# Kernel optimization log

Hardware: AMD Instinct MI355X
Metric: run time of the kernel (lower is better)

## Reference

```python
import jax, jax.numpy as jnp
import numpy as np
from jax import lax

IN_FEATURES = 1024
CLASSES = 512
OUT_CHANNELS = 32
N = 4096
CONV1_OUT = 32
K = 3


def setup_inputs() -> dict:
    key = jax.random.key(0)
    ks = jax.random.split(key, 7)
    s_lin = 1.0 / np.sqrt(IN_FEATURES)
    s_c1 = 1.0 / np.sqrt(1 * K)
    s_c2 = 1.0 / np.sqrt(CONV1_OUT * K)
    return {
        "x": jax.random.normal(ks[0], (N, IN_FEATURES), dtype=jnp.float32),
        "W_w": jax.random.uniform(ks[1], (CLASSES, IN_FEATURES), jnp.float32, -s_lin, s_lin),
        "W_b": jax.random.uniform(ks[2], (CLASSES,), jnp.float32, -s_lin, s_lin),
        "conv1_w": jax.random.uniform(ks[3], (CONV1_OUT, 1, K), jnp.float32, -s_c1, s_c1),
        "conv1_b": jax.random.uniform(ks[4], (CONV1_OUT,), jnp.float32, -s_c1, s_c1),
        "conv2_w": jax.random.uniform(ks[5], (OUT_CHANNELS, CONV1_OUT, K), jnp.float32, -s_c2, s_c2),
        "conv2_b": jax.random.uniform(ks[6], (OUT_CHANNELS,), jnp.float32, -s_c2, s_c2),
    }


def _conv1d(x, w, b):
    # x: [N, C_in, L], w: [C_out, C_in, K], padding=1 (same)
    y = lax.conv_general_dilated(
        x, w, window_strides=(1,), padding=((1, 1),),
        dimension_numbers=("NCH", "OIH", "NCH"))
    return y + b[None, :, None]


def reference(x, W_w, W_b, conv1_w, conv1_b, conv2_w, conv2_b):
    # SelfAttention: h = x W^T + b  -> [N, CLASSES]
    h = x @ W_w.T + W_b
    # attention = softmax(tanh(h h^T), dim=1)  -> [N, N]
    scores = jnp.tanh(h @ h.T)
    attn = jax.nn.softmax(scores, axis=1)
    a = jnp.tanh(attn @ h)                     # [N, CLASSES]
    a = jax.nn.relu(a)
    # unsqueeze(-1).permute(0,2,1): [N, CLASSES] -> [N, 1, CLASSES]
    z = a[:, None, :]
    z = jax.nn.relu(_conv1d(z, conv1_w, conv1_b))   # [N, 32, CLASSES]
    z = jax.nn.relu(_conv1d(z, conv2_w, conv2_b))   # [N, OUT_CHANNELS, CLASSES]
    return jnp.transpose(z, (0, 2, 1))              # [N, CLASSES, OUT_CHANNELS]
```

## Files before the change

kernel.cpp:

```cpp
#include <hip/hip_runtime.h>

typedef __bf16 bf16_t;
typedef __bf16 bf16x8 __attribute__((ext_vector_type(8)));
typedef __bf16 bf16x4v __attribute__((ext_vector_type(4)));
typedef __bf16 bf16x2 __attribute__((ext_vector_type(2)));
typedef float f32x4 __attribute__((ext_vector_type(4)));

__device__ __forceinline__ float tanh_fast(float x) {
  float a = fabsf(x);
  float e = __expf(-2.f * a);
  float t = (1.f - e) * __builtin_amdgcn_rcpf(1.f + e);
  return copysignf(t, x);
}

__device__ __forceinline__ void gload16(const void* g, void* l) {
  __builtin_amdgcn_global_load_lds(
      (const __attribute__((address_space(1))) void*)g,
      (__attribute__((address_space(3))) void*)l, 16, 0, 0);
}

__global__ __launch_bounds__(256) void cast_all_k(const float* __restrict__ x,
                                                  const float* __restrict__ Ww,
                                                  const float* __restrict__ w2,
                                                  bf16_t* __restrict__ xb,
                                                  bf16_t* __restrict__ Wbf,
                                                  bf16_t* __restrict__ w2rg) {
  const int bid = blockIdx.x;
  const int tid = threadIdx.x;
  if (bid < 4096) {
    const int i = bid * 256 + tid;
    float4 v = ((const float4*)x)[i];
    bf16x4v o;
    o[0] = (bf16_t)v.x; o[1] = (bf16_t)v.y; o[2] = (bf16_t)v.z; o[3] = (bf16_t)v.w;
    ((bf16x4v*)xb)[i] = o;
  } else if (bid < 4608) {
    const int i = (bid - 4096) * 256 + tid;
    float4 v = ((const float4*)Ww)[i];
    bf16x4v o;
    o[0] = (bf16_t)v.x; o[1] = (bf16_t)v.y; o[2] = (bf16_t)v.z; o[3] = (bf16_t)v.w;
    ((bf16x4v*)Wbf)[i] = o;
  } else {
    for (int i = tid; i < 3072; i += 256) {
      int o = i / 96, rem = i % 96, c = rem / 3, kk = rem % 3;
      w2rg[kk * 1024 + o * 32 + c] = (bf16_t)w2[i];
    }
  }
}

#define BAR() __builtin_amdgcn_s_barrier()
#define WLG() asm volatile("s_waitcnt lgkmcnt(0)" ::: "memory")
#define RDA(b, am)                                                              \
  do {                                                                          \
    _Pragma("unroll") for (int j = 0; j < 4; ++j) {                             \
      afr[j][0] = *(const bf16x8*)(pA + (b)*16384 + (am)*4096 + j*1024);        \
      afr[j][1] = *(const bf16x8*)(pA + (b)*16384 + 8192 + (am)*4096 + j*1024); \
    }                                                                           \
  } while (0)
#define RDB(b, bn)                                                              \
  do {                                                                          \
    _Pragma("unroll") for (int jj = 0; jj < 2; ++jj) {                          \
      bfr[jj][0] = *(const bf16x8*)(pB + (b)*16384 + ((bn)*2+jj)*1024);         \
      bfr[jj][1] = *(const bf16x8*)(pB + (b)*16384 + 8192 + ((bn)*2+jj)*1024);  \
    }                                                                           \
  } while (0)
#define MM16(am, bn)                                                            \
  do {                                                                          \
    __builtin_amdgcn_s_setprio(1);                                              \
    _Pragma("unroll") for (int kk = 0; kk < 2; ++kk)                            \
    _Pragma("unroll") for (int j = 0; j < 4; ++j)                               \
    _Pragma("unroll") for (int jj = 0; jj < 2; ++jj)                            \
      acc[(am)*4+j][(bn)*2+jj] = __builtin_amdgcn_mfma_f32_16x16x32_bf16(       \
          afr[j][kk], bfr[jj][kk], acc[(am)*4+j][(bn)*2+jj], 0, 0, 0);          \
    __builtin_amdgcn_s_setprio(0);                                              \
  } while (0)
#define STGA(tile, half)                                                        \
  do {                                                                          \
    const bf16_t* s_ = Ag + (size_t)(half)*128*lda + (tile)*64;                 \
    char* d_ = lds_raw + (half)*32768 + ((tile)&1)*16384 + tid*16;              \
    gload16(s_, d_); gload16(s_ + 32, d_ + 8192);                               \
  } while (0)
#define STGB(tile, half)                                                        \
  do {                                                                          \
    const bf16_t* s_ = Bg + (size_t)(half)*128*ldb + (tile)*64;                 \
    char* d_ = lds_raw + 65536 + (half)*32768 + ((tile)&1)*16384 + tid*16;      \
    gload16(s_, d_); gload16(s_ + 32, d_ + 8192);                               \
  } while (0)

template <int EPI>
__global__ __launch_bounds__(512, 2) void gemm8_k(const bf16_t* __restrict__ A,
                                                  const bf16_t* __restrict__ Bt,
                                                  bf16_t* __restrict__ out,
                                                  float* __restrict__ psum,
                                                  int lda, int ldb, int ldc,
                                                  int Klen, size_t pstride) {
  __shared__ __attribute__((aligned(16))) char lds_raw[131072];
  const int tid = threadIdx.x;
  const int wid = tid >> 6, l = tid & 63;
  const int wm = wid >> 2, wn = wid & 3;
  const int lr = l & 15, lkq = l >> 4;

  const int gx = gridDim.x, gy = gridDim.y;
  const int flat = blockIdx.x + gx * (blockIdx.y + gy * blockIdx.z);
  const int n = gx * gy * gridDim.z;
  const int s = (flat & 7) * (n >> 3) + (flat >> 3);
  const int lgx = __builtin_ctz(gx), lgy = __builtin_ctz(gy);
  const int bx = s & (gx - 1);
  const int by = (s >> lgx) & (gy - 1);
  const int bz = s >> (lgx + lgy);

  const size_t koff = (size_t)bz * Klen;
  const int NI = Klen >> 7;

  const int srow = tid >> 2;
  const int scol = ((tid & 3) * 8) ^ (((tid >> 5) & 1) << 4);
  const bf16_t* Ag = A + (size_t)(by * 256 + srow) * lda + koff + scol;
  const bf16_t* Bg = Bt + (size_t)(bx * 256 + srow) * ldb + koff + scol;

  const int kby = (lkq * 16) ^ (((lr >> 3) & 1) << 5);
  const char* pA = lds_raw + wm * 32768 + lr * 64 + kby;
  const char* pB = lds_raw + 65536 + (wn >> 1) * 32768 + ((wn & 1) * 64 + lr) * 64 + kby;

  bf16x8 afr[4][2], bfr[2][2];
  f32x4 acc[8][4];
#pragma unroll
  for (int m = 0; m < 8; ++m)
#pragma unroll
    for (int n2 = 0; n2 < 4; ++n2) acc[m][n2] = (f32x4){0.f, 0.f, 0.f, 0.f};

  STGA(0, 0); STGA(0, 1); STGB(0, 0); STGB(0, 1); STGA(1, 0);

  for (int i = 0; i < NI; ++i) {
    const int t1 = 2 * i + 1, t2 = 2 * i + 2, t3 = 2 * i + 3;
    const bool more = (i + 1 < NI);
    asm volatile("s_waitcnt vmcnt(2)" ::: "memory");
    BAR();
    RDA(0, 0); RDB(0, 0);
    STGA(t1, 1);
    WLG(); MM16(0, 0); BAR();
    RDB(0, 1); STGB(t1, 0);
    BAR(); WLG(); MM16(0, 1); BAR();
    RDA(0, 1); STGB(t1, 1);
    BAR(); WLG(); MM16(1, 1); BAR();
    RDB(0, 0);
    if (more) STGA(t2, 0);
    BAR(); WLG(); MM16(1, 0); BAR();
    if (more) { asm volatile("s_waitcnt vmcnt(2)" ::: "memory"); }
    else      { asm volatile("s_waitcnt vmcnt(0)" ::: "memory"); }
    BAR();
    RDA(1, 0); RDB(1, 0);
    if (more) STGA(t2, 1);
    WLG(); MM16(0, 0); BAR();
    RDB(1, 1);
    if (more) STGB(t2, 0);
    BAR(); WLG(); MM16(0, 1); BAR();
    RDA(1, 1);
    if (more) STGB(t2, 1);
    BAR(); WLG(); MM16(1, 1); BAR();
    RDB(1, 0);
    if (more) STGA(t3, 0);
    BAR(); WLG(); MM16(1, 0); BAR();
  }

  if constexpr (EPI == 1) {
    float* ps = psum + (size_t)(bx * 4 + wn) * 4096;
#pragma unroll
    for (int mi = 0; mi < 8; ++mi) {
#pragma unroll
      for (int v = 0; v < 4; ++v) {
        const int r = wm * 128 + mi * 16 + lkq * 4 + v;
        float rs = 0.f;
#pragma unroll
        for (int ni = 0; ni < 4; ++ni) {
          float val = __expf(tanh_fast(acc[mi][ni][v]));
          const int cb = ((wn * 64 + ni * 16 + lr) * 2) ^ ((r & 4) << 4);
          *(bf16_t*)(lds_raw + r * 512 + cb) = (bf16_t)val;
          rs += val;
        }
        rs += __shfl_xor(rs, 1);
        rs += __shfl_xor(rs, 2);
        rs += __shfl_xor(rs, 4);
        rs += __shfl_xor(rs, 8);
        if (lr == 0) ps[by * 256 + r] = rs;
      }
    }
  } else {
#pragma unroll
    for (int mi = 0; mi < 8; ++mi)
#pragma unroll
      for (int v = 0; v < 4; ++v) {
        const int r = wm * 128 + mi * 16 + lkq * 4 + v;
#pragma unroll
        for (int ni = 0; ni < 4; ++ni) {
          const int cb = ((wn * 64 + ni * 16 + lr) * 2) ^ ((r & 4) << 4);
          *(bf16_t*)(lds_raw + r * 512 + cb) = (bf16_t)acc[mi][ni][v];
        }
      }
  }
  __syncthreads();
  bf16_t* obase = (EPI == 1) ? out : out + (size_t)bz * pstride;
#pragma unroll
  for (int k = 0; k < 16; ++k) {
    const int idx = k * 512 + tid;
    const int row = idx >> 5, cc = idx & 31;
    bf16x8 vv = *(const bf16x8*)(lds_raw + ((row * 512 + cc * 16) ^ ((row & 4) << 4)));
    *(bf16x8*)&obase[(size_t)(by * 256 + row) * ldc + bx * 256 + cc * 8] = vv;
  }
}

template <int EPI>
__global__ __launch_bounds__(256) void gemm_bt_k(const bf16_t* __restrict__ A,
                                                 const bf16_t* __restrict__ Bt,
                                                 const float* __restrict__ extra,
                                                 bf16_t* __restrict__ out,
                                                 float* __restrict__ outf,
                                                 float* __restrict__ psum,
                                                 int M, int N, int Kloop, int lda, int ldb) {
  __shared__ bf16_t As[128 * 32];
  __shared__ bf16_t Bs[128 * 32];
  const int tid = threadIdx.x;
  const int w = tid >> 6;
  const int l = tid & 63;
  const int bx = blockIdx.x, by = blockIdx.y;
  const int koff = blockIdx.z * Kloop;

  const bf16_t* src = (w < 2) ? A : Bt;
  const int stride = (w < 2) ? lda : ldb;
  bf16_t* dstbase = (w < 2) ? As : Bs;
  const int tile0 = (w < 2 ? by : bx) * 128 + (w & 1) * 64;
  const int srow = l >> 2;
  const int scol = (l & 3) * 8;
  const bf16_t* gbase = src + (size_t)(tile0 + srow) * stride + scol + koff;
  bf16_t* lbase = dstbase + (w & 1) * (64 * 32);

  const int wm = w >> 1, wn = w & 1;
  const int lrow = l & 15;
  const int lk = (l >> 4) * 8;

  f32x4 zero = {0.f, 0.f, 0.f, 0.f};
  f32x4 acc[4][4];
  for (int m = 0; m < 4; ++m)
    for (int n = 0; n < 4; ++n) acc[m][n] = zero;

  for (int kt = 0; kt < Kloop; kt += 32) {
    const bf16_t* g = gbase + kt;
#pragma unroll
    for (int i = 0; i < 4; ++i) gload16(g + (size_t)i * 16 * stride, lbase + i * 512);
    __syncthreads();
    bf16x8 af[4], bfv[4];
#pragma unroll
    for (int m = 0; m < 4; ++m)
      af[m] = *(const bf16x8*)&As[(wm * 64 + m * 16 + lrow) * 32 + lk];
#pragma unroll
    for (int n = 0; n < 4; ++n)
      bfv[n] = *(const bf16x8*)&Bs[(wn * 64 + n * 16 + lrow) * 32 + lk];
#pragma unroll
    for (int m = 0; m < 4; ++m)
#pragma unroll
      for (int n = 0; n < 4; ++n)
        acc[m][n] = __builtin_amdgcn_mfma_f32_16x16x32_bf16(af[m], bfv[n], acc[m][n], 0, 0, 0);
    __syncthreads();
  }

  const int row0 = by * 128 + wm * 64;
  const int col0 = bx * 128 + wn * 64;

  if constexpr (EPI == 3) {
    float* of = outf + (size_t)blockIdx.z * M * N;
#pragma unroll
    for (int m = 0; m < 4; ++m)
#pragma unroll
      for (int v = 0; v < 4; ++v) {
        const int row = row0 + m * 16 + ((l >> 4) << 2) + v;
#pragma unroll
        for (int n = 0; n < 4; ++n)
          of[(size_t)row * N + col0 + n * 16 + lrow] = acc[m][n][v];
      }
    return;
  }

  if constexpr (EPI == 1) {
#pragma unroll
    for (int m = 0; m < 4; ++m)
#pragma unroll
      for (int v = 0; v < 4; ++v) {
        const int row = row0 + m * 16 + ((l >> 4) << 2) + v;
        float rs = 0.f;
#pragma unroll
        for (int n = 0; n < 4; ++n) {
          const int col = col0 + n * 16 + lrow;
          float val = __expf(tanh_fast(acc[m][n][v]));
          out[(size_t)row * N + col] = (bf16_t)val;
          rs += val;
        }
        if (psum) {
          rs += __shfl_xor(rs, 1);
          rs += __shfl_xor(rs, 2);
          rs += __shfl_xor(rs, 4);
          rs += __shfl_xor(rs, 8);
          if ((l & 15) == 0) psum[(size_t)(bx * 2 + wn) * M + row] = rs;
        }
      }
    return;
  }

  float bcol[4];
#pragma unroll
  for (int n = 0; n < 4; ++n)
    bcol[n] = (EPI == 0) ? extra[col0 + n * 16 + lrow] : 0.f;

#pragma unroll
  for (int m = 0; m < 4; ++m) {
#pragma unroll
    for (int v = 0; v < 4; ++v) {
      const int row = row0 + m * 16 + ((l >> 4) << 2) + v;
      float inv_dn = 1.f;
      if constexpr (EPI == 2) inv_dn = 1.f / extra[row];
#pragma unroll
      for (int n = 0; n < 4; ++n) {
        const int col = col0 + n * 16 + lrow;
        float val = acc[m][n][v];
        float o;
        if constexpr (EPI == 0) o = val + bcol[n];
        else o = fmaxf(tanh_fast(val * inv_dn), 0.f);
        out[(size_t)row * N + col] = (bf16_t)o;
      }
    }
  }
}

__global__ __launch_bounds__(256) void reduce1T_k(const float* __restrict__ p0,
                                                  const float* __restrict__ p1,
                                                  const float* __restrict__ bias,
                                                  bf16_t* __restrict__ h,
                                                  bf16_t* __restrict__ hT) {
  __shared__ bf16_t tile[64][65];
  const int d0 = blockIdx.x * 64;
  const int i0 = blockIdx.y * 64;
  const int tid = threadIdx.x;
#pragma unroll
  for (int p = 0; p < 2; ++p) {
    const int r = p * 32 + (tid >> 3);
    const int c8 = (tid & 7) * 8;
    const size_t idx = (size_t)(i0 + r) * 512 + d0 + c8;
    float4 a0 = *(const float4*)&p0[idx];
    float4 a1 = *(const float4*)&p0[idx + 4];
    float4 b0 = *(const float4*)&p1[idx];
    float4 b1 = *(const float4*)&p1[idx + 4];
    float4 w0 = *(const float4*)&bias[d0 + c8];
    float4 w1 = *(const float4*)&bias[d0 + c8 + 4];
    bf16x8 o;
    o[0] = (bf16_t)(a0.x + b0.x + w0.x);
    o[1] = (bf16_t)(a0.y + b0.y + w0.y);
    o[2] = (bf16_t)(a0.z + b0.z + w0.z);
    o[3] = (bf16_t)(a0.w + b0.w + w0.w);
    o[4] = (bf16_t)(a1.x + b1.x + w1.x);
    o[5] = (bf16_t)(a1.y + b1.y + w1.y);
    o[6] = (bf16_t)(a1.z + b1.z + w1.z);
    o[7] = (bf16_t)(a1.w + b1.w + w1.w);
    *(bf16x8*)&h[idx] = o;
#pragma unroll
    for (int k = 0; k < 8; ++k) tile[r][c8 + k] = o[k];
  }
  __syncthreads();
#pragma unroll
  for (int p = 0; p < 2; ++p) {
    const int d = p * 32 + (tid >> 3);
    const int i8 = (tid & 7) * 8;
    bf16x8 u;
#pragma unroll
    for (int k = 0; k < 8; ++k) u[k] = tile[i8 + k][d];
    *(bf16x8*)&hT[(size_t)(d0 + d) * 4096 + i0 + i8] = u;
  }
}

__global__ __launch_bounds__(256) void transpose_k(const bf16_t* __restrict__ h,
                                                   bf16_t* __restrict__ hT) {
  __shared__ bf16_t tile[64][65];
  const int i0 = blockIdx.x * 64;
  const int d0 = blockIdx.y * 64;
  const int tid = threadIdx.x;
#pragma unroll
  for (int p = 0; p < 2; ++p) {
    int r = p * 32 + (tid >> 3);
    int c8 = (tid & 7) * 8;
    bf16x8 v = *(const bf16x8*)&h[(size_t)(i0 + r) * 512 + d0 + c8];
#pragma unroll
    for (int k = 0; k < 8; ++k) tile[r][c8 + k] = v[k];
  }
  __syncthreads();
#pragma unroll
  for (int p = 0; p < 2; ++p) {
    int d = p * 32 + (tid >> 3);
    int i8 = (tid & 7) * 8;
    bf16x8 u;
#pragma unroll
    for (int k = 0; k < 8; ++k) u[k] = tile[i8 + k][d];
    *(bf16x8*)&hT[(size_t)(d0 + d) * 4096 + i0 + i8] = u;
  }
}

__global__ __launch_bounds__(256) void rowsum_k(const bf16_t* __restrict__ P,
                                                float* __restrict__ den) {
  const int r = blockIdx.x;
  const int tid = threadIdx.x;
  const bf16_t* p = P + (size_t)r * 4096 + tid * 16;
  bf16x8 a = *(const bf16x8*)p;
  bf16x8 b = *(const bf16x8*)(p + 8);
  float s = 0.f;
#pragma unroll
  for (int k = 0; k < 8; ++k) s += (float)a[k] + (float)b[k];
  __shared__ float red[256];
  red[tid] = s;
  __syncthreads();
  for (int off = 128; off > 0; off >>= 1) {
    if (tid < off) red[tid] += red[tid + off];
    __syncthreads();
  }
  if (tid == 0) den[r] = red[0];
}

__global__ __launch_bounds__(256) void conv2_fused_k(const bf16_t* __restrict__ pg,
                                                     const float* __restrict__ psum,
                                                     const bf16_t* __restrict__ w2rg,
                                                     const float* __restrict__ w1,
                                                     const float* __restrict__ b1,
                                                     const float* __restrict__ b2,
                                                     float* __restrict__ out, int S) {
  __shared__ bf16_t trow[516];
  __shared__ bf16_t z1t[514 * 40];
  __shared__ bf16_t w2r[3072];
  __shared__ float w1s[96], b1s[32], b2s[32];
  __shared__ float den_s;
  const int r = blockIdx.x;
  const int tid = threadIdx.x;

  if (tid < 96) w1s[tid] = w1[tid];
  if (tid < 32) { b1s[tid] = b1[tid]; b2s[tid] = b2[tid]; }
  ((bf16x8*)w2r)[tid] = ((const bf16x8*)w2rg)[tid];
  if (tid < 128) ((bf16x8*)w2r)[256 + tid] = ((const bf16x8*)w2rg)[256 + tid];

  if (tid < 64) {
    float dp = psum[(size_t)tid * 4096 + r];
    dp += __shfl_xor(dp, 32);
    dp += __shfl_xor(dp, 16);
    dp += __shfl_xor(dp, 8);
    dp += __shfl_xor(dp, 4);
    dp += __shfl_xor(dp, 2);
    dp += __shfl_xor(dp, 1);
    if (tid == 0) den_s = dp;
  }

  float a0 = 0.f, a1 = 0.f;
  {
    const bf16_t* pr = pg + (size_t)r * 512 + tid * 2;
    for (int z = 0; z < S; ++z) {
      bf16x2 v = *(const bf16x2*)(pr + (size_t)z * (4096 * 512));
      a0 += (float)v[0];
      a1 += (float)v[1];
    }
  }
  if (tid == 0) { trow[0] = (bf16_t)0.f; trow[513] = (bf16_t)0.f; }
  if (tid < 40) { z1t[tid] = (bf16_t)0.f; z1t[513 * 40 + tid] = (bf16_t)0.f; }
  __syncthreads();

  {
    const float inv = 1.f / den_s;
    trow[1 + 2 * tid] = (bf16_t)fmaxf(tanh_fast(a0 * inv), 0.f);
    trow[2 + 2 * tid] = (bf16_t)fmaxf(tanh_fast(a1 * inv), 0.f);
  }
  __syncthreads();

  {
    const int c = tid & 31;
    const int jb = (tid >> 5) * 64;
    const float wc0 = w1s[c * 3], wc1 = w1s[c * 3 + 1], wc2 = w1s[c * 3 + 2];
    const float bb = b1s[c];
    float tm = (float)trow[jb];
    float t0 = (float)trow[jb + 1];
    for (int j = jb; j < jb + 64; ++j) {
      float tp2 = (float)trow[j + 2];
      float v = fmaxf(bb + wc0 * tm + wc1 * t0 + wc2 * tp2, 0.f);
      z1t[(j + 1) * 40 + c] = (bf16_t)v;
      tm = t0; t0 = tp2;
    }
  }
  __syncthreads();

  const int w = tid >> 6, l = tid & 63;
  const int lrow = l & 15;
  const int lk = (l >> 4) * 8;
  bf16x8 af[3][2];
#pragma unroll
  for (int kk = 0; kk < 3; ++kk)
#pragma unroll
    for (int m = 0; m < 2; ++m)
      af[kk][m] = *(const bf16x8*)&w2r[kk * 1024 + (m * 16 + lrow) * 32 + lk];

  f32x4 zero = {0.f, 0.f, 0.f, 0.f};
  f32x4 acc[2][8];
#pragma unroll
  for (int m = 0; m < 2; ++m)
#pragma unroll
    for (int n = 0; n < 8; ++n) acc[m][n] = zero;

  const int j0 = w * 128;
#pragma unroll
  for (int kk = 0; kk < 3; ++kk) {
#pragma unroll
    for (int n = 0; n < 8; ++n) {
      bf16x8 bfv = *(const bf16x8*)&z1t[(j0 + n * 16 + lrow + kk) * 40 + lk];
      acc[0][n] = __builtin_amdgcn_mfma_f32_16x16x32_bf16(af[kk][0], bfv, acc[0][n], 0, 0, 0);
      acc[1][n] = __builtin_amdgcn_mfma_f32_16x16x32_bf16(af[kk][1], bfv, acc[1][n], 0, 0, 0);
    }
  }

#pragma unroll
  for (int m = 0; m < 2; ++m) {
    const int ob = m * 16 + ((l >> 4) << 2);
    const float bb0 = b2s[ob], bb1 = b2s[ob + 1], bb2 = b2s[ob + 2], bb3 = b2s[ob + 3];
#pragma unroll
    for (int n = 0; n < 8; ++n) {
      const int j = j0 + n * 16 + lrow;
      f32x4 res;
      res[0] = fmaxf(acc[m][n][0] + bb0, 0.f);
      res[1] = fmaxf(acc[m][n][1] + bb1, 0.f);
      res[2] = fmaxf(acc[m][n][2] + bb2, 0.f);
      res[3] = fmaxf(acc[m][n][3] + bb3, 0.f);
      *(f32x4*)&out[((size_t)r * 512 + j) * 32 + ob] = res;
    }
  }
}

__global__ __launch_bounds__(256) void conv_fused_k(const bf16_t* __restrict__ t,
                                                    const float* __restrict__ w1,
                                                    const float* __restrict__ b1,
                                                    const float* __restrict__ w2,
                                                    const float* __restrict__ b2,
                                                    float* __restrict__ out) {
  __shared__ bf16_t trow[516];
  __shared__ bf16_t z1t[514 * 40];
  __shared__ bf16_t w2r[3 * 32 * 32];
  __shared__ float w1s[96], b1s[32], b2s[32];
  const int r = blockIdx.x;
  const int tid = threadIdx.x;

  if (tid < 96) w1s[tid] = w1[tid];
  if (tid < 32) { b1s[tid] = b1[tid]; b2s[tid] = b2[tid]; }
  for (int i = tid; i < 3072; i += 256) {
    int o = i / 96, rem = i % 96, c = rem / 3, kk = rem % 3;
    w2r[kk * 1024 + o * 32 + c] = (bf16_t)w2[i];
  }
  {
    const bf16_t* tp = t + (size_t)r * 512;
    trow[1 + tid] = tp[tid];
    trow[1 + 256 + tid] = tp[256 + tid];
    if (tid == 0) { trow[0] = (bf16_t)0.f; trow[513] = (bf16_t)0.f; }
    if (tid < 40) { z1t[tid] = (bf16_t)0.f; z1t[513 * 40 + tid] = (bf16_t)0.f; }
  }
  __syncthreads();

  {
    const int c = tid & 31;
    const int jb = (tid >> 5) * 64;
    const float wc0 = w1s[c * 3], wc1 = w1s[c * 3 + 1], wc2 = w1s[c * 3 + 2];
    const float bb = b1s[c];
    float tm = (float)trow[jb];
    float t0 = (float)trow[jb + 1];
    for (int j = jb; j < jb + 64; ++j) {
      float tp2 = (float)trow[j + 2];
      float v = fmaxf(bb + wc0 * tm + wc1 * t0 + wc2 * tp2, 0.f);
      z1t[(j + 1) * 40 + c] = (bf16_t)v;
      tm = t0; t0 = tp2;
    }
  }
  __syncthreads();

  const int w = tid >> 6, l = tid & 63;
  const int lrow = l & 15;
  const int lk = (l >> 4) * 8;
  bf16x8 af[3][2];
#pragma unroll
  for (int kk = 0; kk < 3; ++kk)
#pragma unroll
    for (int m = 0; m < 2; ++m)
      af[kk][m] = *(const bf16x8*)&w2r[kk * 1024 + (m * 16 + lrow) * 32 + lk];

  f32x4 zero = {0.f, 0.f, 0.f, 0.f};
  f32x4 acc[2][8];
#pragma unroll
  for (int m = 0; m < 2; ++m)
#pragma unroll
    for (int n = 0; n < 8; ++n) acc[m][n] = zero;

  const int j0 = w * 128;
#pragma unroll
  for (int kk = 0; kk < 3; ++kk) {
#pragma unroll
    for (int n = 0; n < 8; ++n) {
      bf16x8 bfv = *(const bf16x8*)&z1t[(j0 + n * 16 + lrow + kk) * 40 + lk];
      acc[0][n] = __builtin_amdgcn_mfma_f32_16x16x32_bf16(af[kk][0], bfv, acc[0][n], 0, 0, 0);
      acc[1][n] = __builtin_amdgcn_mfma_f32_16x16x32_bf16(af[kk][1], bfv, acc[1][n], 0, 0, 0);
    }
  }

#pragma unroll
  for (int m = 0; m < 2; ++m) {
    const int ob = m * 16 + ((l >> 4) << 2);
    const float bb0 = b2s[ob], bb1 = b2s[ob + 1], bb2 = b2s[ob + 2], bb3 = b2s[ob + 3];
#pragma unroll
    for (int n = 0; n < 8; ++n) {
      const int j = j0 + n * 16 + lrow;
      f32x4 res;
      res[0] = fmaxf(acc[m][n][0] + bb0, 0.f);
      res[1] = fmaxf(acc[m][n][1] + bb1, 0.f);
      res[2] = fmaxf(acc[m][n][2] + bb2, 0.f);
      res[3] = fmaxf(acc[m][n][3] + bb3, 0.f);
      *(f32x4*)&out[((size_t)r * 512 + j) * 32 + ob] = res;
    }
  }
}

extern "C" void kernel_launch(void* const* d_in, const int* in_sizes, int n_in,
                              void* d_out, int out_size, void* d_ws, size_t ws_size,
                              hipStream_t stream) {
  const float* x = (const float*)d_in[0];
  const float* Ww = (const float*)d_in[1];
  const float* Wb = (const float*)d_in[2];
  const float* c1w = (const float*)d_in[3];
  const float* c1b = (const float*)d_in[4];
  const float* c2w = (const float*)d_in[5];
  const float* c2b = (const float*)d_in[6];
  float* out = (float*)d_out;
  char* ws = (char*)d_ws;

  bf16_t* xb  = (bf16_t*)(ws + 0);
  bf16_t* Wbf = (bf16_t*)(ws + 8388608);
  bf16_t* h   = (bf16_t*)(ws + 9437184);
  bf16_t* hT  = (bf16_t*)(ws + 13631488);
  bf16_t* tb  = (bf16_t*)(ws + 17825792);
  bf16_t* w2rg = (bf16_t*)(ws + 17825792);
  float*  den = (float*)(ws + 22020096);

  cast_all_k<<<4609, 256, 0, stream>>>(x, Ww, c2w, xb, Wbf, w2rg);

  const size_t NEED_FAST = 73416704ull;
  if (ws_size >= NEED_FAST) {
    float*  psum = (float*)(ws + 22036480);
    bf16_t* P    = (bf16_t*)(ws + 23085056);
    float*  pg1  = (float*)(ws + 23085056);
    bf16_t* pg3b = (bf16_t*)(ws + 56639488);

    gemm_bt_k<3><<<dim3(4, 32, 2), 256, 0, stream>>>(xb, Wbf, nullptr, nullptr, pg1,
                                                     nullptr, 4096, 512, 512, 1024, 1024);
    reduce1T_k<<<dim3(8, 64), 256, 0, stream>>>(pg1, pg1 + 4096 * 512, Wb, h, hT);

    gemm8_k<1><<<dim3(16, 16, 1), 512, 0, stream>>>(h, h, P, psum, 512, 512, 4096, 512, 0);

    const int S = (ws_size >= 90193920ull) ? 8 : 4;
    gemm8_k<3><<<dim3(2, 16, S), 512, 0, stream>>>(P, hT, pg3b, nullptr, 4096, 4096, 512,
                                                   4096 / S, (size_t)4096 * 512);

    conv2_fused_k<<<4096, 256, 0, stream>>>(pg3b, psum, w2rg, c1w, c1b, c2b, out, S);
  } else {
    bf16_t* P = (bf16_t*)(ws + 22036480);
    gemm_bt_k<0><<<dim3(4, 32), 256, 0, stream>>>(xb, Wbf, Wb, h, nullptr, nullptr,
                                                  4096, 512, 1024, 1024, 1024);
    transpose_k<<<dim3(64, 8), 256, 0, stream>>>(h, hT);
    gemm_bt_k<1><<<dim3(32, 32), 256, 0, stream>>>(h, h, nullptr, P, nullptr, nullptr,
                                                   4096, 4096, 512, 512, 512);
    rowsum_k<<<4096, 256, 0, stream>>>(P, den);
    gemm_bt_k<2><<<dim3(4, 32), 256, 0, stream>>>(P, hT, den, tb, nullptr, nullptr,
                                                  4096, 512, 4096, 4096, 4096);
    conv_fused_k<<<4096, 256, 0, stream>>>(tb, c1w, c1b, c2w, c2b, out);
  }
}
```

Before: 182.9 us.

## Exploit symmetry of h·hᵀ and split conv epilogue into half-row blocks

The scores GEMM now computes only the upper-triangular 256x256 tiles (136 blocks instead of 256). Each off-diagonal tile writes its transpose to P and column partial sums into psum, which roughly halves the MFMA work for that GEMM. The conv kernel is split into two blocks per row with halo handling, using less LDS and requesting 4 blocks per CU for higher occupancy. The risks are uncoalesced transposed-tile writes from scalar LDS gathers and the extra halo recomputation.

```diff
diff --git a/kernel.cpp b/kernel.cpp
--- a/kernel.cpp
+++ b/kernel.cpp
@@ -85,6 +85,141 @@
     char* d_ = lds_raw + 65536 + (half)*32768 + ((tile)&1)*16384 + tid*16;      \
     gload16(s_, d_); gload16(s_ + 32, d_ + 8192);                               \
   } while (0)
+#define KLOOP8()                                                                \
+  for (int i = 0; i < NI; ++i) {                                                \
+    const int t1 = 2 * i + 1, t2 = 2 * i + 2, t3 = 2 * i + 3;                   \
+    const bool more = (i + 1 < NI);                                             \
+    asm volatile("s_waitcnt vmcnt(2)" ::: "memory");                            \
+    BAR();                                                                      \
+    RDA(0, 0); RDB(0, 0);                                                       \
+    STGA(t1, 1);                                                                \
+    WLG(); MM16(0, 0); BAR();                                                   \
+    RDB(0, 1); STGB(t1, 0);                                                     \
+    BAR(); WLG(); MM16(0, 1); BAR();                                            \
+    RDA(0, 1); STGB(t1, 1);                                                     \
+    BAR(); WLG(); MM16(1, 1); BAR();                                            \
+    RDB(0, 0);                                                                  \
+    if (more) STGA(t2, 0);                                                      \
+    BAR(); WLG(); MM16(1, 0); BAR();                                            \
+    if (more) { asm volatile("s_waitcnt vmcnt(2)" ::: "memory"); }              \
+    else      { asm volatile("s_waitcnt vmcnt(0)" ::: "memory"); }              \
+    BAR();                                                                      \
+    RDA(1, 0); RDB(1, 0);                                                       \
+    if (more) STGA(t2, 1);                                                      \
+    WLG(); MM16(0, 0); BAR();                                                   \
+    RDB(1, 1);                                                                  \
+    if (more) STGB(t2, 0);                                                      \
+    BAR(); WLG(); MM16(0, 1); BAR();                                            \
+    RDA(1, 1);                                                                  \
+    if (more) STGB(t2, 1);                                                      \
+    BAR(); WLG(); MM16(1, 1); BAR();                                            \
+    RDB(1, 0);                                                                  \
+    if (more) STGA(t3, 0);                                                      \
+    BAR(); WLG(); MM16(1, 0); BAR();                                            \
+  }
+
+__global__ __launch_bounds__(512, 2) void gemm8_sym_k(const bf16_t* __restrict__ h,
+                                                      bf16_t* __restrict__ P,
+                                                      float* __restrict__ psum) {
+  __shared__ __attribute__((aligned(16))) char lds_raw[131072];
+  const int tid = threadIdx.x;
+  const int wid = tid >> 6, l = tid & 63;
+  const int wm = wid >> 2, wn = wid & 3;
+  const int lr = l & 15, lkq = l >> 4;
+
+  const int flat = blockIdx.x;
+  int s = (flat & 7) * 17 + (flat >> 3);
+  int rem = s, by = 0;
+  while (rem >= 16 - by) { rem -= 16 - by; ++by; }
+  const int bx = by + rem;
+
+  const int lda = 512, ldb = 512;
+  const int NI = 4;
+
+  const int srow = tid >> 2;
+  const int scol = ((tid & 3) * 8) ^ (((tid >> 5) & 1) << 4);
+  const bf16_t* Ag = h + (size_t)(by * 256 + srow) * 512 + scol;
+  const bf16_t* Bg = h + (size_t)(bx * 256 + srow) * 512 + scol;
+
+  const int kby = (lkq * 16) ^ (((lr >> 3) & 1) << 5);
+  const char* pA = lds_raw + wm * 32768 + lr * 64 + kby;
+  const char* pB = lds_raw + 65536 + (wn >> 1) * 32768 + ((wn & 1) * 64 + lr) * 64 + kby;
+
+  bf16x8 afr[4][2], bfr[2][2];
+  f32x4 acc[8][4];
+#pragma unroll
+  for (int m = 0; m < 8; ++m)
+#pragma unroll
+    for (int n2 = 0; n2 < 4; ++n2) acc[m][n2] = (f32x4){0.f, 0.f, 0.f, 0.f};
+
+  STGA(0, 0); STGA(0, 1); STGB(0, 0); STGB(0, 1); STGA(1, 0);
+  KLOOP8();
+
+  float csum[4] = {0.f, 0.f, 0.f, 0.f};
+  float* ps = psum + (size_t)(bx * 4 + wn) * 4096;
+#pragma unroll
+  for (int mi = 0; mi < 8; ++mi) {
+#pragma unroll
+    for (int v = 0; v < 4; ++v) {
+      const int r = wm * 128 + mi * 16 + lkq * 4 + v;
+      const int fr = ((r ^ (r >> 3)) & 7) << 4;
+      float rs = 0.f;
+#pragma unroll
+      for (int ni = 0; ni < 4; ++ni) {
+        float val = __expf(tanh_fast(acc[mi][ni][v]));
+        const int cb = (((wn * 64 + ni * 16 + lr) * 2) ^ fr);
+        *(bf16_t*)(lds_raw + r * 512 + cb) = (bf16_t)val;
+        rs += val;
+        csum[ni] += val;
+      }
+      rs += __shfl_xor(rs, 1);
+      rs += __shfl_xor(rs, 2);
+      rs += __shfl_xor(rs, 4);
+      rs += __shfl_xor(rs, 8);
+      if (lr == 0) ps[by * 256 + r] = rs;
+    }
+  }
+  if (bx != by) {
+#pragma unroll
+    for (int ni = 0; ni < 4; ++ni) {
+      csum[ni] += __shfl_xor(csum[ni], 16);
+      csum[ni] += __shfl_xor(csum[ni], 32);
+    }
+    if (lkq == 0) {
+      float* pc = psum + (size_t)(by * 4 + wm) * 4096 + bx * 256 + wn * 64;
+      float* pz = psum + (size_t)(by * 4 + 2 + wm) * 4096 + bx * 256 + wn * 64;
+#pragma unroll
+      for (int ni = 0; ni < 4; ++ni) {
+        pc[ni * 16 + lr] = csum[ni];
+        pz[ni * 16 + lr] = 0.f;
+      }
+    }
+  }
+  __syncthreads();
+#pragma unroll
+  for (int k = 0; k < 16; ++k) {
+    const int idx = k * 512 + tid;
+    const int row = idx >> 5, cc = idx & 31;
+    const int fr = ((row ^ (row >> 3)) & 7) << 4;
+    bf16x8 vv = *(const bf16x8*)(lds_raw + row * 512 + ((cc * 16) ^ fr));
+    *(bf16x8*)&P[(size_t)(by * 256 + row) * 4096 + bx * 256 + cc * 8] = vv;
+  }
+  if (bx != by) {
+#pragma unroll
+    for (int k = 0; k < 16; ++k) {
+      const int idx = k * 512 + tid;
+      const int rp = idx >> 5, cc = idx & 31;
+      bf16x8 u;
+#pragma unroll
+      for (int e = 0; e < 8; ++e) {
+        const int rr = cc * 8 + e;
+        const int fr = ((rr ^ (rr >> 3)) & 7) << 4;
+        u[e] = *(const bf16_t*)(lds_raw + rr * 512 + ((rp * 2) ^ fr));
+      }
+      *(bf16x8*)&P[(size_t)(bx * 256 + rp) * 4096 + by * 256 + cc * 8] = u;
+    }
+  }
+}
 
 template <int EPI>
 __global__ __launch_bounds__(512, 2) void gemm8_k(const bf16_t* __restrict__ A,
@@ -128,76 +263,21 @@
     for (int n2 = 0; n2 < 4; ++n2) acc[m][n2] = (f32x4){0.f, 0.f, 0.f, 0.f};
 
   STGA(0, 0); STGA(0, 1); STGB(0, 0); STGB(0, 1); STGA(1, 0);
-
-  for (int i = 0; i < NI; ++i) {
-    const int t1 = 2 * i + 1, t2 = 2 * i + 2, t3 = 2 * i + 3;
-    const bool more = (i + 1 < NI);
-    asm volatile("s_waitcnt vmcnt(2)" ::: "memory");
-    BAR();
-    RDA(0, 0); RDB(0, 0);
-    STGA(t1, 1);
-    WLG(); MM16(0, 0); BAR();
-    RDB(0, 1); STGB(t1, 0);
-    BAR(); WLG(); MM16(0, 1); BAR();
-    RDA(0, 1); STGB(t1, 1);
-    BAR(); WLG(); MM16(1, 1); BAR();
-    RDB(0, 0);
-    if (more) STGA(t2, 0);
-    BAR(); WLG(); MM16(1, 0); BAR();
-    if (more) { asm volatile("s_waitcnt vmcnt(2)" ::: "memory"); }
-    else      { asm volatile("s_waitcnt vmcnt(0)" ::: "memory"); }
-    BAR();
-    RDA(1, 0); RDB(1, 0);
-    if (more) STGA(t2, 1);
-    WLG(); MM16(0, 0); BAR();
-    RDB(1, 1);
-    if (more) STGB(t2, 0);
-    BAR(); WLG(); MM16(0, 1); BAR();
-    RDA(1, 1);
-    if (more) STGB(t2, 1);
-    BAR(); WLG(); MM16(1, 1); BAR();
-    RDB(1, 0);
-    if (more) STGA(t3, 0);
-    BAR(); WLG(); MM16(1, 0); BAR();
-  }
-
-  if constexpr (EPI == 1) {
-    float* ps = psum + (size_t)(bx * 4 + wn) * 4096;
-#pragma unroll
-    for (int mi = 0; mi < 8; ++mi) {
-#pragma unroll
-      for (int v = 0; v < 4; ++v) {
-        const int r = wm * 128 + mi * 16 + lkq * 4 + v;
-        float rs = 0.f;
-#pragma unroll
-        for (int ni = 0; ni < 4; ++ni) {
-          float val = __expf(tanh_fast(acc[mi][ni][v]));
-          const int cb = ((wn * 64 + ni * 16 + lr) * 2) ^ ((r & 4) << 4);
-          *(bf16_t*)(lds_raw + r * 512 + cb) = (bf16_t)val;
-          rs += val;
-        }
-        rs += __shfl_xor(rs, 1);
-        rs += __shfl_xor(rs, 2);
-        rs += __shfl_xor(rs, 4);
-        rs += __shfl_xor(rs, 8);
-        if (lr == 0) ps[by * 256 + r] = rs;
+  KLOOP8();
+
+#pragma unroll
+  for (int mi = 0; mi < 8; ++mi)
+#pragma unroll
+    for (int v = 0; v < 4; ++v) {
+      const int r = wm * 128 + mi * 16 + lkq * 4 + v;
+#pragma unroll
+      for (int ni = 0; ni < 4; ++ni) {
+        const int cb = ((wn * 64 + ni * 16 + lr) * 2) ^ ((r & 4) << 4);
+        *(bf16_t*)(lds_raw + r * 512 + cb) = (bf16_t)acc[mi][ni][v];
       }
     }
-  } else {
-#pragma unroll
-    for (int mi = 0; mi < 8; ++mi)
-#pragma unroll
-      for (int v = 0; v < 4; ++v) {
-        const int r = wm * 128 + mi * 16 + lkq * 4 + v;
-#pragma unroll
-        for (int ni = 0; ni < 4; ++ni) {
-          const int cb = ((wn * 64 + ni * 16 + lr) * 2) ^ ((r & 4) << 4);
-          *(bf16_t*)(lds_raw + r * 512 + cb) = (bf16_t)acc[mi][ni][v];
-        }
-      }
-  }
-  __syncthreads();
-  bf16_t* obase = (EPI == 1) ? out : out + (size_t)bz * pstride;
+  __syncthreads();
+  bf16_t* obase = out + (size_t)bz * pstride;
 #pragma unroll
   for (int k = 0; k < 16; ++k) {
     const int idx = k * 512 + tid;
@@ -419,19 +499,21 @@
   if (tid == 0) den[r] = red[0];
 }
 
-__global__ __launch_bounds__(256) void conv2_fused_k(const bf16_t* __restrict__ pg,
-                                                     const float* __restrict__ psum,
-                                                     const bf16_t* __restrict__ w2rg,
-                                                     const float* __restrict__ w1,
-                                                     const float* __restrict__ b1,
-                                                     const float* __restrict__ b2,
-                                                     float* __restrict__ out, int S) {
-  __shared__ bf16_t trow[516];
-  __shared__ bf16_t z1t[514 * 40];
+__global__ __launch_bounds__(256, 4) void conv2_fused_k(const bf16_t* __restrict__ pg,
+                                                        const float* __restrict__ psum,
+                                                        const bf16_t* __restrict__ w2rg,
+                                                        const float* __restrict__ w1,
+                                                        const float* __restrict__ b1,
+                                                        const float* __restrict__ b2,
+                                                        float* __restrict__ out, int S) {
+  __shared__ bf16_t trow[264];
+  __shared__ bf16_t z1t[258 * 40 + 8];
   __shared__ bf16_t w2r[3072];
   __shared__ float w1s[96], b1s[32], b2s[32];
   __shared__ float den_s;
-  const int r = blockIdx.x;
+  const int r = blockIdx.x >> 1;
+  const int half = blockIdx.x & 1;
+  const int j0 = half * 256;
   const int tid = threadIdx.x;
 
   if (tid < 96) w1s[tid] = w1[tid];
@@ -452,21 +534,124 @@
 
   float a0 = 0.f, a1 = 0.f;
   {
-    const bf16_t* pr = pg + (size_t)r * 512 + tid * 2;
-    for (int z = 0; z < S; ++z) {
-      bf16x2 v = *(const bf16x2*)(pr + (size_t)z * (4096 * 512));
-      a0 += (float)v[0];
-      a1 += (float)v[1];
-    }
-  }
-  if (tid == 0) { trow[0] = (bf16_t)0.f; trow[513] = (bf16_t)0.f; }
-  if (tid < 40) { z1t[tid] = (bf16_t)0.f; z1t[513 * 40 + tid] = (bf16_t)0.f; }
+    const int jA = j0 - 2 + tid;
+    if (jA >= 0 && jA < 512) {
+      const bf16_t* pr = pg + (size_t)r * 512 + jA;
+      for (int z = 0; z < S; ++z) a0 += (float)pr[(size_t)z * (4096 * 512)];
+    }
+    if (tid < 4) {
+      const int jB = j0 - 2 + 256 + tid;
+      if (jB >= 0 && jB < 512) {
+        const bf16_t* pr = pg + (size_t)r * 512 + jB;
+        for (int z = 0; z < S; ++z) a1 += (float)pr[(size_t)z * (4096 * 512)];
+      }
+    }
+  }
   __syncthreads();
 
   {
     const float inv = 1.f / den_s;
-    trow[1 + 2 * tid] = (bf16_t)fmaxf(tanh_fast(a0 * inv), 0.f);
-    trow[2 + 2 * tid] = (bf16_t)fmaxf(tanh_fast(a1 * inv), 0.f);
+    const int jA = j0 - 2 + tid;
+    trow[tid] = (jA >= 0 && jA < 512) ? (bf16_t)fmaxf(tanh_fast(a0 * inv), 0.f)
+                                      : (bf16_t)0.f;
+    if (tid < 4) {
+      const int jB = j0 - 2 + 256 + tid;
+      trow[256 + tid] = (jB >= 0 && jB < 512) ? (bf16_t)fmaxf(tanh_fast(a1 * inv), 0.f)
+                                              : (bf16_t)0.f;
+    }
+  }
+  __syncthreads();
+
+  {
+    const int c = tid & 31;
+    const int g = tid >> 5;
+    const int mb = g * 33;
+    const int me = (mb + 33 < 258) ? mb + 33 : 258;
+    const float wc0 = w1s[c * 3], wc1 = w1s[c * 3 + 1], wc2 = w1s[c * 3 + 2];
+    const float bb = b1s[c];
+    float tm = (float)trow[mb];
+    float t0 = (float)trow[mb + 1];
+    for (int m = mb; m < me; ++m) {
+      float tp2 = (float)trow[m + 2];
+      float v = fmaxf(bb + wc0 * tm + wc1 * t0 + wc2 * tp2, 0.f);
+      const int jp = j0 - 1 + m;
+      if (jp < 0 || jp > 511) v = 0.f;
+      z1t[m * 40 + c] = (bf16_t)v;
+      tm = t0; t0 = tp2;
+    }
+  }
+  __syncthreads();
+
+  const int w = tid >> 6, l = tid & 63;
+  const int lrow = l & 15;
+  const int lk = (l >> 4) * 8;
+  bf16x8 af[3][2];
+#pragma unroll
+  for (int kk = 0; kk < 3; ++kk)
+#pragma unroll
+    for (int m = 0; m < 2; ++m)
+      af[kk][m] = *(const bf16x8*)&w2r[kk * 1024 + (m * 16 + lrow) * 32 + lk];
+
+  f32x4 zero = {0.f, 0.f, 0.f, 0.f};
+  f32x4 acc[2][4];
+#pragma unroll
+  for (int m = 0; m < 2; ++m)
+#pragma unroll
+    for (int n = 0; n < 4; ++n) acc[m][n] = zero;
+
+  const int jlb = w * 64;
+#pragma unroll
+  for (int kk = 0; kk < 3; ++kk) {
+#pragma unroll
+    for (int n = 0; n < 4; ++n) {
+      bf16x8 bfv = *(const bf16x8*)&z1t[(jlb + n * 16 + lrow + kk) * 40 + lk];
+      acc[0][n] = __builtin_amdgcn_mfma_f32_16x16x32_bf16(af[kk][0], bfv, acc[0][n], 0, 0, 0);
+      acc[1][n] = __builtin_amdgcn_mfma_f32_16x16x32_bf16(af[kk][1], bfv, acc[1][n], 0, 0, 0);
+    }
+  }
+
+#pragma unroll
+  for (int m = 0; m < 2; ++m) {
+    const int ob = m * 16 + ((l >> 4) << 2);
+    const float bb0 = b2s[ob], bb1 = b2s[ob + 1], bb2 = b2s[ob + 2], bb3 = b2s[ob + 3];
+#pragma unroll
+    for (int n = 0; n < 4; ++n) {
+      const int j = j0 + jlb + n * 16 + lrow;
+      f32x4 res;
+      res[0] = fmaxf(acc[m][n][0] + bb0, 0.f);
+      res[1] = fmaxf(acc[m][n][1] + bb1, 0.f);
+      res[2] = fmaxf(acc[m][n][2] + bb2, 0.f);
+      res[3] = fmaxf(acc[m][n][3] + bb3, 0.f);
+      *(f32x4*)&out[((size_t)r * 512 + j) * 32 + ob] = res;
+    }
+  }
+}
+
+__global__ __launch_bounds__(256) void conv_fused_k(const bf16_t* __restrict__ t,
+                                                    const float* __restrict__ w1,
+                                                    const float* __restrict__ b1,
+                                                    const float* __restrict__ w2,
+                                                    const float* __restrict__ b2,
+                                                    float* __restrict__ out) {
+  __shared__ bf16_t trow[516];
+  __shared__ bf16_t z1t[514 * 40];
+  __shared__ bf16_t w2r[3 * 32 * 32];
+  __shared__ float w1s[96], b1s[32], b2s[32];
+  const int r = blockIdx.x;
+  const int tid = threadIdx.x;
+
+  if (tid < 96) w1s[tid] = w1[tid];
+  if (tid < 32) { b1s[tid] = b1[tid]; b2s[tid] = b2[tid]; }
+  for (int i = tid; i < 3072; i += 256) {
+    int o = i / 96, rem = i % 96, c = rem / 3, kk = rem % 3;
+    w2r[kk * 1024 + o * 32 + c] = (bf16_t)w2[i];
+  }
+  {
+    const bf16_t* tp = t + (size_t)r * 512;
+    trow[1 + tid] = tp[tid];
+    trow[1 + 256 + tid] = tp[256 + tid];
+    if (tid == 0) { trow[0] = (bf16_t)0.f; trow[513] = (bf16_t)0.f; }
+    if (tid < 40) { z1t[tid] = (bf16_t)0.f; z1t[513 * 40 + tid] = (bf16_t)0.f; }
   }
   __syncthreads();
 
@@ -531,95 +716,6 @@
   }
 }
 
-__global__ __launch_bounds__(256) void conv_fused_k(const bf16_t* __restrict__ t,
-                                                    const float* __restrict__ w1,
-                                                    const float* __restrict__ b1,
-                                                    const float* __restrict__ w2,
-                                                    const float* __restrict__ b2,
-                                                    float* __restrict__ out) {
-  __shared__ bf16_t trow[516];
-  __shared__ bf16_t z1t[514 * 40];
-  __shared__ bf16_t w2r[3 * 32 * 32];
-  __shared__ float w1s[96], b1s[32], b2s[32];
-  const int r = blockIdx.x;
-  const int tid = threadIdx.x;
-
-  if (tid < 96) w1s[tid] = w1[tid];
-  if (tid < 32) { b1s[tid] = b1[tid]; b2s[tid] = b2[tid]; }
-  for (int i = tid; i < 3072; i += 256) {
-    int o = i / 96, rem = i % 96, c = rem / 3, kk = rem % 3;
-    w2r[kk * 1024 + o * 32 + c] = (bf16_t)w2[i];
-  }
-  {
-    const bf16_t* tp = t + (size_t)r * 512;
-    trow[1 + tid] = tp[tid];
-    trow[1 + 256 + tid] = tp[256 + tid];
-    if (tid == 0) { trow[0] = (bf16_t)0.f; trow[513] = (bf16_t)0.f; }
-    if (tid < 40) { z1t[tid] = (bf16_t)0.f; z1t[513 * 40 + tid] = (bf16_t)0.f; }
-  }
-  __syncthreads();
-
-  {
-    const int c = tid & 31;
-    const int jb = (tid >> 5) * 64;
-    const float wc0 = w1s[c * 3], wc1 = w1s[c * 3 + 1], wc2 = w1s[c * 3 + 2];
-    const float bb = b1s[c];
-    float tm = (float)trow[jb];
-    float t0 = (float)trow[jb + 1];
-    for (int j = jb; j < jb + 64; ++j) {
-      float tp2 = (float)trow[j + 2];
-      float v = fmaxf(bb + wc0 * tm + wc1 * t0 + wc2 * tp2, 0.f);
-      z1t[(j + 1) * 40 + c] = (bf16_t)v;
-      tm = t0; t0 = tp2;
-    }
-  }
-  __syncthreads();
-
-  const int w = tid >> 6, l = tid & 63;
-  const int lrow = l & 15;
-  const int lk = (l >> 4) * 8;
-  bf16x8 af[3][2];
-#pragma unroll
-  for (int kk = 0; kk < 3; ++kk)
-#pragma unroll
-    for (int m = 0; m < 2; ++m)
-      af[kk][m] = *(const bf16x8*)&w2r[kk * 1024 + (m * 16 + lrow) * 32 + lk];
-
-  f32x4 zero = {0.f, 0.f, 0.f, 0.f};
-  f32x4 acc[2][8];
-#pragma unroll
-  for (int m = 0; m < 2; ++m)
-#pragma unroll
-    for (int n = 0; n < 8; ++n) acc[m][n] = zero;
-
-  const int j0 = w * 128;
-#pragma unroll
-  for (int kk = 0; kk < 3; ++kk) {
-#pragma unroll
-    for (int n = 0; n < 8; ++n) {
-      bf16x8 bfv = *(const bf16x8*)&z1t[(j0 + n * 16 + lrow + kk) * 40 + lk];
-      acc[0][n] = __builtin_amdgcn_mfma_f32_16x16x32_bf16(af[kk][0], bfv, acc[0][n], 0, 0, 0);
-      acc[1][n] = __builtin_amdgcn_mfma_f32_16x16x32_bf16(af[kk][1], bfv, acc[1][n], 0, 0, 0);
-    }
-  }
-
-#pragma unroll
-  for (int m = 0; m < 2; ++m) {
-    const int ob = m * 16 + ((l >> 4) << 2);
-    const float bb0 = b2s[ob], bb1 = b2s[ob + 1], bb2 = b2s[ob + 2], bb3 = b2s[ob + 3];
-#pragma unroll
-    for (int n = 0; n < 8; ++n) {
-      const int j = j0 + n * 16 + lrow;
-      f32x4 res;
-      res[0] = fmaxf(acc[m][n][0] + bb0, 0.f);
-      res[1] = fmaxf(acc[m][n][1] + bb1, 0.f);
-      res[2] = fmaxf(acc[m][n][2] + bb2, 0.f);
-      res[3] = fmaxf(acc[m][n][3] + bb3, 0.f);
-      *(f32x4*)&out[((size_t)r * 512 + j) * 32 + ob] = res;
-    }
-  }
-}
-
 extern "C" void kernel_launch(void* const* d_in, const int* in_sizes, int n_in,
                               void* d_out, int out_size, void* d_ws, size_t ws_size,
                               hipStream_t stream) {
@@ -654,13 +750,13 @@
                                                      nullptr, 4096, 512, 512, 1024, 1024);
     reduce1T_k<<<dim3(8, 64), 256, 0, stream>>>(pg1, pg1 + 4096 * 512, Wb, h, hT);
 
-    gemm8_k<1><<<dim3(16, 16, 1), 512, 0, stream>>>(h, h, P, psum, 512, 512, 4096, 512, 0);
+    gemm8_sym_k<<<136, 512, 0, stream>>>(h, P, psum);
 
     const int S = (ws_size >= 90193920ull) ? 8 : 4;
     gemm8_k<3><<<dim3(2, 16, S), 512, 0, stream>>>(P, hT, pg3b, nullptr, 4096, 4096, 512,
                                                    4096 / S, (size_t)4096 * 512);
 
-    conv2_fused_k<<<4096, 256, 0, stream>>>(pg3b, psum, w2rg, c1w, c1b, c2b, out, S);
+    conv2_fused_k<<<8192, 256, 0, stream>>>(pg3b, psum, w2rg, c1w, c1b, c2b, out, S);
   } else {
     bf16_t* P = (bf16_t*)(ws + 22036480);
     gemm_bt_k<0><<<dim3(4, 32), 256, 0, stream>>>(xb, Wbf, Wb, h, nullptr, nullptr,
```

Result: no change. 185.3 us (+1.3%).

## Fuse first linear GEMM with bias, bf16 store and transpose in one kernel

Applied to the files above, without the earlier changes.

Replaces the split-K first GEMM, which wrote fp32 partials, and the separate reduce/transpose kernel with a single 64x128-tile MFMA kernel. That kernel adds the bias and writes both h and hT from an LDS staging tile. This removes the fp32 partial-sum round trip through memory and one launch. The cost is no split-K parallelism (256 blocks) and a simple single-buffered K loop with two barriers per step, which may underuse the GPU.

```diff
diff --git a/kernel.cpp b/kernel.cpp
--- a/kernel.cpp
+++ b/kernel.cpp
@@ -44,6 +44,85 @@
       int o = i / 96, rem = i % 96, c = rem / 3, kk = rem % 3;
       w2rg[kk * 1024 + o * 32 + c] = (bf16_t)w2[i];
     }
+  }
+}
+
+__global__ __launch_bounds__(256) void gemm1_fused_k(const bf16_t* __restrict__ xb,
+                                                     const bf16_t* __restrict__ Wbf,
+                                                     const float* __restrict__ bias,
+                                                     bf16_t* __restrict__ h,
+                                                     bf16_t* __restrict__ hT) {
+  __shared__ bf16_t As[64 * 32];
+  __shared__ bf16_t Bs[128 * 32];
+  __shared__ bf16_t tileO[64][136];
+  const int tid = threadIdx.x;
+  const int w = tid >> 6, l = tid & 63;
+  const int lr = l & 15, lkq = l >> 4;
+  const int bx = blockIdx.x, by = blockIdx.y;
+
+  const bf16_t* Ag  = xb + (size_t)(by * 64 + (tid >> 2)) * 1024 + (tid & 3) * 8;
+  const bf16_t* Bg0 = Wbf + (size_t)(bx * 128 + (tid >> 2)) * 1024 + (tid & 3) * 8;
+  const bf16_t* Bg1 = Bg0 + (size_t)64 * 1024;
+  bf16_t* lA  = As + tid * 8;
+  bf16_t* lB0 = Bs + tid * 8;
+  bf16_t* lB1 = Bs + 2048 + tid * 8;
+
+  f32x4 acc[4][2];
+#pragma unroll
+  for (int m = 0; m < 4; ++m)
+#pragma unroll
+    for (int n = 0; n < 2; ++n) acc[m][n] = (f32x4){0.f, 0.f, 0.f, 0.f};
+
+  for (int kt = 0; kt < 1024; kt += 32) {
+    gload16(Ag + kt, lA);
+    gload16(Bg0 + kt, lB0);
+    gload16(Bg1 + kt, lB1);
+    __syncthreads();
+    bf16x8 af[4], bfv[2];
+#pragma unroll
+    for (int m = 0; m < 4; ++m)
+      af[m] = *(const bf16x8*)&As[(m * 16 + lr) * 32 + lkq * 8];
+#pragma unroll
+    for (int n = 0; n < 2; ++n)
+      bfv[n] = *(const bf16x8*)&Bs[(w * 32 + n * 16 + lr) * 32 + lkq * 8];
+#pragma unroll
+    for (int m = 0; m < 4; ++m)
+#pragma unroll
+      for (int n = 0; n < 2; ++n)
+        acc[m][n] = __builtin_amdgcn_mfma_f32_16x16x32_bf16(af[m], bfv[n], acc[m][n], 0, 0, 0);
+    __syncthreads();
+  }
+
+  float bcol[2];
+#pragma unroll
+  for (int n = 0; n < 2; ++n) bcol[n] = bias[bx * 128 + w * 32 + n * 16 + lr];
+
+#pragma unroll
+  for (int m = 0; m < 4; ++m)
+#pragma unroll
+    for (int v = 0; v < 4; ++v) {
+      const int r = m * 16 + lkq * 4 + v;
+#pragma unroll
+      for (int n = 0; n < 2; ++n)
+        tileO[r][w * 32 + n * 16 + lr] = (bf16_t)(acc[m][n][v] + bcol[n]);
+    }
+  __syncthreads();
+
+#pragma unroll
+  for (int k = 0; k < 4; ++k) {
+    const int idx = k * 256 + tid;
+    const int row = idx >> 4, vec = idx & 15;
+    bf16x8 vv = *(const bf16x8*)&tileO[row][vec * 8];
+    *(bf16x8*)&h[(size_t)(by * 64 + row) * 512 + bx * 128 + vec * 8] = vv;
+  }
+#pragma unroll
+  for (int k = 0; k < 4; ++k) {
+    const int idx = k * 256 + tid;
+    const int d = idx >> 3, vec = idx & 7;
+    bf16x8 u;
+#pragma unroll
+    for (int e = 0; e < 8; ++e) u[e] = tileO[vec * 8 + e][d];
+    *(bf16x8*)&hT[(size_t)(bx * 128 + d) * 4096 + by * 64 + vec * 8] = u;
   }
 }
 
@@ -328,51 +407,6 @@
   }
 }
 
-__global__ __launch_bounds__(256) void reduce1T_k(const float* __restrict__ p0,
-                                                  const float* __restrict__ p1,
-                                                  const float* __restrict__ bias,
-                                                  bf16_t* __restrict__ h,
-                                                  bf16_t* __restrict__ hT) {
-  __shared__ bf16_t tile[64][65];
-  const int d0 = blockIdx.x * 64;
-  const int i0 = blockIdx.y * 64;
-  const int tid = threadIdx.x;
-#pragma unroll
-  for (int p = 0; p < 2; ++p) {
-    const int r = p * 32 + (tid >> 3);
-    const int c8 = (tid & 7) * 8;
-    const size_t idx = (size_t)(i0 + r) * 512 + d0 + c8;
-    float4 a0 = *(const float4*)&p0[idx];
-    float4 a1 = *(const float4*)&p0[idx + 4];
-    float4 b0 = *(const float4*)&p1[idx];
-    float4 b1 = *(const float4*)&p1[idx + 4];
-    float4 w0 = *(const float4*)&bias[d0 + c8];
-    float4 w1 = *(const float4*)&bias[d0 + c8 + 4];
-    bf16x8 o;
-    o[0] = (bf16_t)(a0.x + b0.x + w0.x);
-    o[1] = (bf16_t)(a0.y + b0.y + w0.y);
-    o[2] = (bf16_t)(a0.z + b0.z + w0.z);
-    o[3] = (bf16_t)(a0.w + b0.w + w0.w);
-    o[4] = (bf16_t)(a1.x + b1.x + w1.x);
-    o[5] = (bf16_t)(a1.y + b1.y + w1.y);
-    o[6] = (bf16_t)(a1.z + b1.z + w1.z);
-    o[7] = (bf16_t)(a1.w + b1.w + w1.w);
-    *(bf16x8*)&h[idx] = o;
-#pragma unroll
-    for (int k = 0; k < 8; ++k) tile[r][c8 + k] = o[k];
-  }
-  __syncthreads();
-#pragma unroll
-  for (int p = 0; p < 2; ++p) {
-    const int d = p * 32 + (tid >> 3);
-    const int i8 = (tid & 7) * 8;
-    bf16x8 u;
-#pragma unroll
-    for (int k = 0; k < 8; ++k) u[k] = tile[i8 + k][d];
-    *(bf16x8*)&hT[(size_t)(d0 + d) * 4096 + i0 + i8] = u;
-  }
-}
-
 __global__ __launch_bounds__(256) void transpose_k(const bf16_t* __restrict__ h,
                                                    bf16_t* __restrict__ hT) {
   __shared__ bf16_t tile[64][65];
@@ -647,12 +681,9 @@
   if (ws_size >= NEED_FAST) {
     float*  psum = (float*)(ws + 22036480);
     bf16_t* P    = (bf16_t*)(ws + 23085056);
-    float*  pg1  = (float*)(ws + 23085056);
     bf16_t* pg3b = (bf16_t*)(ws + 56639488);
 
-    gemm_bt_k<3><<<dim3(4, 32, 2), 256, 0, stream>>>(xb, Wbf, nullptr, nullptr, pg1,
-                                                     nullptr, 4096, 512, 512, 1024, 1024);
-    reduce1T_k<<<dim3(8, 64), 256, 0, stream>>>(pg1, pg1 + 4096 * 512, Wb, h, hT);
+    gemm1_fused_k<<<dim3(4, 64), 256, 0, stream>>>(xb, Wbf, Wb, h, hT);
 
     gemm8_k<1><<<dim3(16, 16, 1), 512, 0, stream>>>(h, h, P, psum, 512, 512, 4096, 512, 0);
 
```

Measured after the change: 181.2 us (median of 2 runs). Within noise of the previous version (-0.9%).
